# Kernel tuning notes

Measured on AMD Instinct MI355X. Metric: run time of the kernel, lower is better.

## Reference

```python
import jax, jax.numpy as jnp
import numpy as np

H = 1024  # latent_dim / GRU hidden size


def setup_inputs() -> dict:
    key = jax.random.key(0)
    ks = jax.random.split(key, 7)
    B, T, E, V = 16, 256, 512, 32000
    return {
        "latent_samples": jax.random.normal(ks[0], (B, H), jnp.float32),
        "true_outputs": jax.random.normal(ks[1], (B, T, E), jnp.float32),
        "gru_kernel": jax.random.normal(ks[2], (E, 3 * H), jnp.float32) * 0.02,
        "gru_rec_kernel": jax.random.normal(ks[3], (H, 3 * H), jnp.float32) * 0.02,
        "gru_bias": jax.random.normal(ks[4], (2, 3 * H), jnp.float32) * 0.02,
        "dense_w": jax.random.normal(ks[5], (H, V), jnp.float32) * 0.02,
        "dense_b": jax.random.normal(ks[6], (V,), jnp.float32) * 0.02,
    }


def reference(latent_samples, true_outputs, gru_kernel, gru_rec_kernel, gru_bias, dense_w, dense_b):
    # teacher_forcing_decode: GRU over true_outputs[:, :-1, :] with initial state latent_samples,
    # then TimeDistributed Dense to vocab logits. Keras GRU, reset_after=True, gate order z|r|h.
    teacher = true_outputs[:, :-1, :]                      # [B, T-1, E]
    # Precompute all input projections at once: [B, T-1, 3H]
    x_proj = jnp.einsum('bte,eg->btg', teacher, gru_kernel) + gru_bias[0]
    rec_bias = gru_bias[1]

    def step(h, x_t):  # h: [B,H], x_t: [B,3H]
        rec = h @ gru_rec_kernel + rec_bias              # [B,3H]
        xz, xr, xh = jnp.split(x_t, 3, axis=-1)
        rz, rr, rh = jnp.split(rec, 3, axis=-1)
        z = jax.nn.sigmoid(xz + rz)
        r = jax.nn.sigmoid(xr + rr)
        hh = jnp.tanh(xh + r * rh)
        h_new = z * h + (1.0 - z) * hh
        return h_new, h_new

    _, hs = jax.lax.scan(step, latent_samples, jnp.swapaxes(x_proj, 0, 1))  # hs: [T-1, B, H]
    gru_out = jnp.swapaxes(hs, 0, 1)                       # [B, T-1, H]
    logits = jnp.einsum('bth,hv->btv', gru_out, dense_w) + dense_b
    return logits
```

## Files before the change

kernel.cpp:

```cpp
#include <hip/hip_runtime.h>


typedef __attribute__((ext_vector_type(8))) short s16x8;
typedef __attribute__((ext_vector_type(4))) float f32x4;
typedef __attribute__((ext_vector_type(4))) int   i32x4;

#define B_      16
#define TSTEPS  255
#define H_      1024
#define G_      3072
#define E_      512
#define V_      32000
#define MROWS   4080
#define MPAD    4096
#define NBLK_SCAN 64
#define NWORK     448
#define NBLK_TOT  512
#define NTILE_RB  32
#define NTILE_CB  250
#define FSTRIDE   16
#define NCOPY     8
#define HCPY      16384

__device__ __forceinline__ short f2bf(float f) {
  unsigned u = __float_as_uint(f);
  u = (u + 0x7fffu + ((u >> 16) & 1u)) >> 16;
  return (short)u;
}

__device__ __forceinline__ float frcp(float x) {
  float r;
  asm("v_rcp_f32 %0, %1" : "=v"(r) : "v"(x));
  return r;
}

#define GLD_SC(dst, p)                                                         \
  asm volatile("global_load_dwordx4 %0, %1, off sc0 sc1"                       \
               : "=v"(dst) : "v"(p) : "memory")

__device__ __forceinline__ void gload_lds16(const short* g, void* l) {
  __builtin_amdgcn_global_load_lds((const __attribute__((address_space(1))) void*)g,
                                   (__attribute__((address_space(3))) void*)l,
                                   16, 0, 0);
}


__global__ void transpose_cvt(const float* __restrict__ src, short* __restrict__ dst,
                              int K, int N) {
  __shared__ float tile[32][33];
  const int n0 = blockIdx.x * 32, k0 = blockIdx.y * 32;
  const int tx = threadIdx.x, ty0 = threadIdx.y;
#pragma unroll
  for (int yy = 0; yy < 4; ++yy) {
    int ty = ty0 + yy * 8;
    tile[ty][tx] = src[(size_t)(k0 + ty) * N + (n0 + tx)];
  }
  __syncthreads();
#pragma unroll
  for (int yy = 0; yy < 4; ++yy) {
    int ty = ty0 + yy * 8;
    dst[(size_t)(n0 + ty) * K + (k0 + tx)] = f2bf(tile[tx][ty]);
  }
}

__global__ void pack_teacher(const float* __restrict__ src, short* __restrict__ dst) {
  int idx = blockIdx.x * 256 + threadIdx.x;
  int row = idx >> 6;
  int c8 = (idx & 63) << 3;
  int t = row >> 4, b = row & 15;
  s16x8 v = {};
  if (t < TSTEPS) {
    const float* s = src + ((size_t)(b * 256 + t)) * E_ + c8;
#pragma unroll
    for (int j = 0; j < 8; ++j) v[j] = f2bf(s[j]);
  }
  *(s16x8*)(dst + (size_t)row * E_ + c8) = v;
}

__global__ void init_h(const float* __restrict__ latent, short* __restrict__ hb) {
  int i = blockIdx.x * 256 + threadIdx.x;
  const short v = f2bf(latent[i]);
#pragma unroll
  for (int cp = 0; cp < NCOPY; ++cp) hb[cp * HCPY + i] = v;
}

__global__ __launch_bounds__(256) void gemm_bf16(
    const short* __restrict__ A, const short* __restrict__ BT,
    const float* __restrict__ bias, float* __restrict__ C, int N, int K) {
  const int tid = threadIdx.x;
  const int lane = tid & 63, w = tid >> 6;
  const int r = lane & 15, q = lane >> 4;
  const int bm = blockIdx.y * 128, bn = blockIdx.x * 128;
  const int wm = bm + (w >> 1) * 64, wn = bn + (w & 1) * 64;
  const short* Ab = A + (size_t)(wm + r) * K + q * 8;
  const short* Bb = BT + (size_t)(wn + r) * K + q * 8;
  f32x4 acc[4][4] = {};
  s16x8 a0[4], b0[4], a1[4], b1[4];
  const int nk = K >> 5;
#define GL(AA, BB, kk)                                                         \
  {                                                                            \
    _Pragma("unroll") for (int i = 0; i < 4; ++i) {                            \
      AA[i] = *(const s16x8*)(Ab + (size_t)i * 16 * K + (kk) * 32);            \
    }                                                                          \
    _Pragma("unroll") for (int j = 0; j < 4; ++j) {                            \
      BB[j] = *(const s16x8*)(Bb + (size_t)j * 16 * K + (kk) * 32);            \
    }                                                                          \
  }
#define MM(AA, BB)                                                             \
  {                                                                            \
    _Pragma("unroll") for (int i = 0; i < 4; ++i)                              \
        _Pragma("unroll") for (int j = 0; j < 4; ++j)                          \
            acc[i][j] = __builtin_amdgcn_mfma_f32_16x16x32_bf16(               \
                AA[i], BB[j], acc[i][j], 0, 0, 0);                             \
  }
  GL(a0, b0, 0)
#pragma unroll 1
  for (int ks = 0; ks < nk; ks += 2) {
    GL(a1, b1, ks + 1)
    MM(a0, b0)
    if (ks + 2 < nk) GL(a0, b0, ks + 2)
    MM(a1, b1)
  }
#undef GL
#undef MM
#pragma unroll
  for (int j = 0; j < 4; ++j) {
    const int col = wn + j * 16 + r;
    const float bv = bias[col];
#pragma unroll
    for (int i = 0; i < 4; ++i) {
#pragma unroll
      for (int rr = 0; rr < 4; ++rr) {
        const int row = wm + i * 16 + q * 4 + rr;
        C[(size_t)row * N + col] = acc[i][j][rr] + bv;
      }
    }
  }
}

__global__ __launch_bounds__(256, 2) void fused_scan_gemm(
    const short* __restrict__ WrecT,
    const float* __restrict__ xproj,
    const float* __restrict__ bias1,
    const float* __restrict__ latent,
    short* __restrict__ hbuf,
    short* __restrict__ gruout,
    const short* __restrict__ DwT,
    const float* __restrict__ db,
    float* __restrict__ out,
    unsigned* __restrict__ sync) {
  const int tid = threadIdx.x, lane = tid & 63, w = tid >> 6;
  const int r = lane & 15, q = lane >> 4;
  __shared__ s16x8 smem_v[2048];
  unsigned* scanflag = sync;
  unsigned* frontier = sync + NCOPY * 1024;

  if (blockIdx.x < NBLK_SCAN) {
    __builtin_amdgcn_s_setprio(3);
    float (*red)[3][64][4] = (float(*)[3][64][4])smem_v;
    const int c = blockIdx.x;
    const int cp = c & 7;
    s16x8 wb[3][8];
#pragma unroll
    for (int g = 0; g < 3; ++g)
#pragma unroll
      for (int s = 0; s < 8; ++s)
        wb[g][s] = *(const s16x8*)(WrecT + (size_t)(g * 1024 + c * 16 + r) * 1024 +
                                   (w * 8 + s) * 32 + q * 8);

    const int m = tid >> 4, nl = tid & 15, col = c * 16 + nl;
    float h = latent[m * 1024 + col];
    const float bz = bias1[col], brr = bias1[1024 + col], bhh = bias1[2048 + col];
    const float* xb = xproj + (size_t)m * G_;
    float xz = xb[col], xr = xb[1024 + col], xh = xb[2048 + col];

    for (int t = 0; t < TSTEPS; ++t) {
      const short* hcur = hbuf + ((size_t)((t & 1) * NCOPY + cp)) * HCPY;
      unsigned* hnxt = (unsigned*)(hbuf + (size_t)((t & 1) ^ 1) * NCOPY * HCPY);
      i32x4 afi[8];
#pragma unroll
      for (int s = 0; s < 8; ++s)
        GLD_SC(afi[s], hcur + r * 1024 + (w * 8 + s) * 32 + q * 8);
      asm volatile("s_waitcnt vmcnt(0)"
                   : "+v"(afi[0]), "+v"(afi[1]), "+v"(afi[2]), "+v"(afi[3]),
                     "+v"(afi[4]), "+v"(afi[5]), "+v"(afi[6]), "+v"(afi[7])
                   :: "memory");
      __builtin_amdgcn_sched_barrier(0);
      f32x4 acc[3] = {};
#pragma unroll
      for (int s = 0; s < 8; ++s) {
        const s16x8 af = *(const s16x8*)&afi[s];
        acc[0] = __builtin_amdgcn_mfma_f32_16x16x32_bf16(af, wb[0][s], acc[0], 0, 0, 0);
        acc[1] = __builtin_amdgcn_mfma_f32_16x16x32_bf16(af, wb[1][s], acc[1], 0, 0, 0);
        acc[2] = __builtin_amdgcn_mfma_f32_16x16x32_bf16(af, wb[2][s], acc[2], 0, 0, 0);
      }
      *(f32x4*)&red[w][0][lane][0] = acc[0];
      *(f32x4*)&red[w][1][lane][0] = acc[1];
      *(f32x4*)&red[w][2][lane][0] = acc[2];
      __syncthreads();
      const int rl = (m >> 2) * 16 + nl, ri = m & 3;
      float rz = bz, rr2 = brr, rh = bhh;
#pragma unroll
      for (int ww = 0; ww < 4; ++ww) {
        rz += red[ww][0][rl][ri];
        rr2 += red[ww][1][rl][ri];
        rh += red[ww][2][rl][ri];
      }
      const float z = frcp(1.f + __expf(-(xz + rz)));
      const float rg = frcp(1.f + __expf(-(xr + rr2)));
      const float hh = tanhf(xh + rg * rh);
      h = z * h + (1.f - z) * hh;
      const unsigned hb16 = (unsigned short)f2bf(h);
      const unsigned nb = __shfl(hb16, lane | 1, 64);
      const unsigned pv = hb16 | (nb << 16);
      const unsigned hoff = (unsigned)((m * 1024 + col) >> 1);
      if (!(tid & 1)) {
#pragma unroll
        for (int cp2 = 0; cp2 < NCOPY; ++cp2)
          __hip_atomic_store(hnxt + cp2 * (HCPY / 2) + hoff, pv,
                             __ATOMIC_RELAXED, __HIP_MEMORY_SCOPE_AGENT);
      }
      __syncthreads();
      if (tid == 0) {
#pragma unroll
        for (int cp2 = 0; cp2 < NCOPY; ++cp2)
          __hip_atomic_store(&scanflag[cp2 * 1024 + c * FSTRIDE], (unsigned)(t + 1),
                             __ATOMIC_RELAXED, __HIP_MEMORY_SCOPE_AGENT);
      }
      if (!(tid & 1))
        __hip_atomic_store((unsigned*)gruout + (((size_t)(t * 16 + m)) * 1024 + col) / 2,
                           pv, __ATOMIC_RELAXED, __HIP_MEMORY_SCOPE_AGENT);
      if ((t & 7) == 7) {
        asm volatile("s_waitcnt vmcnt(0)" ::: "memory");
        __syncthreads();
        if (tid == 0)
          __hip_atomic_store(&frontier[c * FSTRIDE], (unsigned)(t + 1),
                             __ATOMIC_RELAXED, __HIP_MEMORY_SCOPE_AGENT);
      }
      {
        const float* xn = xb + (size_t)(t + 1) * 16 * G_;
        xz = xn[col]; xr = xn[1024 + col]; xh = xn[2048 + col];
      }
      if (t < TSTEPS - 1) {
        const unsigned* fp = &scanflag[cp * 1024 + lane * FSTRIDE];
        unsigned v = __hip_atomic_load(fp, __ATOMIC_RELAXED,
                                       __HIP_MEMORY_SCOPE_AGENT);
        while (!__all(v > (unsigned)t))
          v = __hip_atomic_load(fp, __ATOMIC_RELAXED, __HIP_MEMORY_SCOPE_AGENT);
      }
    }
    asm volatile("s_waitcnt vmcnt(0)" ::: "memory");
    __syncthreads();
    if (tid == 0)
      __hip_atomic_store(&frontier[c * FSTRIDE], 256u,
                         __ATOMIC_RELAXED, __HIP_MEMORY_SCOPE_AGENT);
  } else {
    char* sb = (char*)smem_v;
    const int wr = w >> 1, wc = w & 1;
    const int xterm = ((q ^ ((r >> 1) & 3)) << 4);
    const int swz8 = (((lane & 3) ^ ((lane >> 3) & 3)) << 3);
    const int j = blockIdx.x - NBLK_SCAN;
#pragma unroll 1
    for (int tq = j; tq < NTILE_RB * NTILE_CB; tq += NWORK) {
      const int rb = tq / NTILE_CB, cb = tq - rb * NTILE_CB;
      const unsigned need = (unsigned)(rb < 31 ? 8 * rb + 8 : 256);
      unsigned v = __hip_atomic_load(&frontier[lane * FSTRIDE], __ATOMIC_RELAXED,
                                     __HIP_MEMORY_SCOPE_AGENT);
      while (!__all(v >= need)) {
        __builtin_amdgcn_s_sleep(32);
        v = __hip_atomic_load(&frontier[lane * FSTRIDE], __ATOMIC_RELAXED,
                              __HIP_MEMORY_SCOPE_AGENT);
      }
      const short* Ag = gruout + (size_t)rb * 128 * 1024;
      const short* Bg = DwT + (size_t)cb * 128 * 1024;
      f32x4 acc[4][4] = {};
#define STAGE(buf, kk)                                                         \
  {                                                                            \
    _Pragma("unroll") for (int it = 0; it < 2; ++it) {                         \
      const size_t go = (size_t)(w * 32 + it * 16 + (lane >> 2)) * 1024 +      \
                        (kk) * 32 + swz8;                                      \
      char* lb2 = sb + (buf) * 16384 + w * 2048 + it * 1024;                   \
      gload_lds16(Ag + go, lb2);                                               \
      gload_lds16(Bg + go, lb2 + 8192);                                        \
    }                                                                          \
  }
      STAGE(0, 0)
#pragma unroll 1
      for (int kk = 0; kk < 32; ++kk) {
        __syncthreads();
        if (kk < 31) STAGE((kk + 1) & 1, kk + 1)
        const char* ab = sb + (kk & 1) * 16384;
        s16x8 af[4], bf[4];
#pragma unroll
        for (int i = 0; i < 4; ++i)
          af[i] = *(const s16x8*)(ab + (wr * 64 + i * 16 + r) * 64 + xterm);
#pragma unroll
        for (int j5 = 0; j5 < 4; ++j5)
          bf[j5] = *(const s16x8*)(ab + 8192 + (wc * 64 + j5 * 16 + r) * 64 + xterm);
#pragma unroll
        for (int i = 0; i < 4; ++i)
#pragma unroll
          for (int j5 = 0; j5 < 4; ++j5)
            acc[i][j5] = __builtin_amdgcn_mfma_f32_16x16x32_bf16(
                af[i], bf[j5], acc[i][j5], 0, 0, 0);
      }
#undef STAGE
      const int wm = rb * 128 + wr * 64, wn = cb * 128 + wc * 64;
#pragma unroll
      for (int j2 = 0; j2 < 4; ++j2) {
        const int col = wn + j2 * 16 + r;
        const float bv = db[col];
#pragma unroll
        for (int i = 0; i < 4; ++i) {
#pragma unroll
          for (int rr = 0; rr < 4; ++rr) {
            const int arow = wm + i * 16 + q * 4 + rr;
            const int t = arow >> 4, mm = arow & 15;
            if (t < TSTEPS)
              __builtin_nontemporal_store(
                  acc[i][j2][rr] + bv,
                  &out[(size_t)(mm * TSTEPS + t) * V_ + col]);
          }
        }
      }
      __syncthreads();
    }
  }
}

extern "C" void kernel_launch(void* const* d_in, const int* in_sizes, int n_in,
                              void* d_out, int out_size, void* d_ws, size_t ws_size,
                              hipStream_t stream) {
  const float* latent = (const float*)d_in[0];
  const float* trueo  = (const float*)d_in[1];
  const float* gk     = (const float*)d_in[2];
  const float* grk    = (const float*)d_in[3];
  const float* gbias  = (const float*)d_in[4];
  const float* dw     = (const float*)d_in[5];
  const float* db     = (const float*)d_in[6];
  float* out = (float*)d_out;
  char* ws = (char*)d_ws;
  short*    WrecT  = (short*)(ws + 0);
  short*    GkT    = (short*)(ws + 6291456);
  short*    DwT    = (short*)(ws + 9437184);
  short*    teachA = (short*)(ws + 74973184);
  short*    hbuf   = (short*)(ws + 74973184);
  unsigned* syncb  = (unsigned*)(ws + 75497472);
  float*    xproj  = (float*)(ws + 79167488);
  short*    gruout = (short*)(ws + 129499136);

  transpose_cvt<<<dim3(96, 32), dim3(32, 8), 0, stream>>>(grk, WrecT, 1024, 3072);
  transpose_cvt<<<dim3(96, 16), dim3(32, 8), 0, stream>>>(gk, GkT, 512, 3072);
  transpose_cvt<<<dim3(1000, 32), dim3(32, 8), 0, stream>>>(dw, DwT, 1024, 32000);
  pack_teacher<<<1024, 256, 0, stream>>>(trueo, teachA);
  gemm_bf16<<<dim3(24, 32), 256, 0, stream>>>(teachA, GkT, gbias, xproj, G_, E_);
  hipMemsetAsync(syncb, 0, 36864, stream);
  init_h<<<64, 256, 0, stream>>>(latent, hbuf);
  fused_scan_gemm<<<NBLK_TOT, 256, 0, stream>>>(WrecT, xproj, gbias + G_, latent,
                                                hbuf, gruout, DwT, db, out, syncb);
}
```

Before: 980.3 us.

## Replace replicated ping-pong hidden-state buffers with a single write-once history buffer

The scan blocks now write each step's hidden state once, to a unique slot in a [T+1,B,H] history buffer. This replaces fanning out to eight replicated ping-pong copies plus eight flag copies and a separate gruout write. Because every address is written only once before it is read, the per-step h loads drop the sc0 sc1 cache-bypass bits, and the logits GEMM reads its A operand straight from the history. The goal is to cut per-step store traffic and latency in the serial recurrence. In exchange, the waitcnt/barrier before publishing the frontier flag is removed, which risks the GEMM blocks seeing the flag before the history writes are visible.

```diff
diff --git a/kernel.cpp b/kernel.cpp
--- a/kernel.cpp
+++ b/kernel.cpp
@@ -19,8 +19,6 @@
 #define NTILE_RB  32
 #define NTILE_CB  250
 #define FSTRIDE   16
-#define NCOPY     8
-#define HCPY      16384
 
 __device__ __forceinline__ short f2bf(float f) {
   unsigned u = __float_as_uint(f);
@@ -34,8 +32,8 @@
   return r;
 }
 
-#define GLD_SC(dst, p)                                                         \
-  asm volatile("global_load_dwordx4 %0, %1, off sc0 sc1"                       \
+#define GLD_C(dst, p)                                                          \
+  asm volatile("global_load_dwordx4 %0, %1, off"                               \
                : "=v"(dst) : "v"(p) : "memory")
 
 __device__ __forceinline__ void gload_lds16(const short* g, void* l) {
@@ -77,11 +75,9 @@
   *(s16x8*)(dst + (size_t)row * E_ + c8) = v;
 }
 
-__global__ void init_h(const float* __restrict__ latent, short* __restrict__ hb) {
+__global__ void init_h(const float* __restrict__ latent, short* __restrict__ hist) {
   int i = blockIdx.x * 256 + threadIdx.x;
-  const short v = f2bf(latent[i]);
-#pragma unroll
-  for (int cp = 0; cp < NCOPY; ++cp) hb[cp * HCPY + i] = v;
+  hist[i] = f2bf(latent[i]);
 }
 
 __global__ __launch_bounds__(256) void gemm_bf16(
@@ -143,8 +139,7 @@
     const float* __restrict__ xproj,
     const float* __restrict__ bias1,
     const float* __restrict__ latent,
-    short* __restrict__ hbuf,
-    short* __restrict__ gruout,
+    short* __restrict__ hist,
     const short* __restrict__ DwT,
     const float* __restrict__ db,
     float* __restrict__ out,
@@ -153,13 +148,12 @@
   const int r = lane & 15, q = lane >> 4;
   __shared__ s16x8 smem_v[2048];
   unsigned* scanflag = sync;
-  unsigned* frontier = sync + NCOPY * 1024;
+  unsigned* frontier = sync + 1024;
 
   if (blockIdx.x < NBLK_SCAN) {
     __builtin_amdgcn_s_setprio(3);
     float (*red)[3][64][4] = (float(*)[3][64][4])smem_v;
     const int c = blockIdx.x;
-    const int cp = c & 7;
     s16x8 wb[3][8];
 #pragma unroll
     for (int g = 0; g < 3; ++g)
@@ -175,12 +169,10 @@
     float xz = xb[col], xr = xb[1024 + col], xh = xb[2048 + col];
 
     for (int t = 0; t < TSTEPS; ++t) {
-      const short* hcur = hbuf + ((size_t)((t & 1) * NCOPY + cp)) * HCPY;
-      unsigned* hnxt = (unsigned*)(hbuf + (size_t)((t & 1) ^ 1) * NCOPY * HCPY);
+      const short* hrow = hist + ((size_t)t * 16 + r) * 1024 + w * 256 + q * 8;
       i32x4 afi[8];
 #pragma unroll
-      for (int s = 0; s < 8; ++s)
-        GLD_SC(afi[s], hcur + r * 1024 + (w * 8 + s) * 32 + q * 8);
+      for (int s = 0; s < 8; ++s) GLD_C(afi[s], hrow + s * 32);
       asm volatile("s_waitcnt vmcnt(0)"
                    : "+v"(afi[0]), "+v"(afi[1]), "+v"(afi[2]), "+v"(afi[3]),
                      "+v"(afi[4]), "+v"(afi[5]), "+v"(afi[6]), "+v"(afi[7])
@@ -213,26 +205,15 @@
       const unsigned hb16 = (unsigned short)f2bf(h);
       const unsigned nb = __shfl(hb16, lane | 1, 64);
       const unsigned pv = hb16 | (nb << 16);
-      const unsigned hoff = (unsigned)((m * 1024 + col) >> 1);
-      if (!(tid & 1)) {
-#pragma unroll
-        for (int cp2 = 0; cp2 < NCOPY; ++cp2)
-          __hip_atomic_store(hnxt + cp2 * (HCPY / 2) + hoff, pv,
-                             __ATOMIC_RELAXED, __HIP_MEMORY_SCOPE_AGENT);
-      }
+      if (!(tid & 1))
+        __hip_atomic_store(
+            (unsigned*)hist + (((size_t)(t + 1) * 16 + m) * 1024 + col) / 2,
+            pv, __ATOMIC_RELAXED, __HIP_MEMORY_SCOPE_AGENT);
       __syncthreads();
-      if (tid == 0) {
-#pragma unroll
-        for (int cp2 = 0; cp2 < NCOPY; ++cp2)
-          __hip_atomic_store(&scanflag[cp2 * 1024 + c * FSTRIDE], (unsigned)(t + 1),
-                             __ATOMIC_RELAXED, __HIP_MEMORY_SCOPE_AGENT);
-      }
-      if (!(tid & 1))
-        __hip_atomic_store((unsigned*)gruout + (((size_t)(t * 16 + m)) * 1024 + col) / 2,
-                           pv, __ATOMIC_RELAXED, __HIP_MEMORY_SCOPE_AGENT);
+      if (tid == 0)
+        __hip_atomic_store(&scanflag[c * FSTRIDE], (unsigned)(t + 1),
+                           __ATOMIC_RELAXED, __HIP_MEMORY_SCOPE_AGENT);
       if ((t & 7) == 7) {
-        asm volatile("s_waitcnt vmcnt(0)" ::: "memory");
-        __syncthreads();
         if (tid == 0)
           __hip_atomic_store(&frontier[c * FSTRIDE], (unsigned)(t + 1),
                              __ATOMIC_RELAXED, __HIP_MEMORY_SCOPE_AGENT);
@@ -242,15 +223,13 @@
         xz = xn[col]; xr = xn[1024 + col]; xh = xn[2048 + col];
       }
       if (t < TSTEPS - 1) {
-        const unsigned* fp = &scanflag[cp * 1024 + lane * FSTRIDE];
+        const unsigned* fp = &scanflag[lane * FSTRIDE];
         unsigned v = __hip_atomic_load(fp, __ATOMIC_RELAXED,
                                        __HIP_MEMORY_SCOPE_AGENT);
         while (!__all(v > (unsigned)t))
           v = __hip_atomic_load(fp, __ATOMIC_RELAXED, __HIP_MEMORY_SCOPE_AGENT);
       }
     }
-    asm volatile("s_waitcnt vmcnt(0)" ::: "memory");
-    __syncthreads();
     if (tid == 0)
       __hip_atomic_store(&frontier[c * FSTRIDE], 256u,
                          __ATOMIC_RELAXED, __HIP_MEMORY_SCOPE_AGENT);
@@ -271,7 +250,7 @@
         v = __hip_atomic_load(&frontier[lane * FSTRIDE], __ATOMIC_RELAXED,
                               __HIP_MEMORY_SCOPE_AGENT);
       }
-      const short* Ag = gruout + (size_t)rb * 128 * 1024;
+      const short* Ag = hist + (size_t)16 * 1024 + (size_t)rb * 128 * 1024;
       const short* Bg = DwT + (size_t)cb * 128 * 1024;
       f32x4 acc[4][4] = {};
 #define STAGE(buf, kk)                                                         \
@@ -344,18 +323,17 @@
   short*    GkT    = (short*)(ws + 6291456);
   short*    DwT    = (short*)(ws + 9437184);
   short*    teachA = (short*)(ws + 74973184);
-  short*    hbuf   = (short*)(ws + 74973184);
-  unsigned* syncb  = (unsigned*)(ws + 75497472);
   float*    xproj  = (float*)(ws + 79167488);
-  short*    gruout = (short*)(ws + 129499136);
-
+  short*    hist   = (short*)(ws + 129499136);
+  unsigned* syncb  = (unsigned*)(ws + 137920512);
+
+  hipMemsetAsync(syncb, 0, 8192, stream);
   transpose_cvt<<<dim3(96, 32), dim3(32, 8), 0, stream>>>(grk, WrecT, 1024, 3072);
   transpose_cvt<<<dim3(96, 16), dim3(32, 8), 0, stream>>>(gk, GkT, 512, 3072);
   transpose_cvt<<<dim3(1000, 32), dim3(32, 8), 0, stream>>>(dw, DwT, 1024, 32000);
   pack_teacher<<<1024, 256, 0, stream>>>(trueo, teachA);
   gemm_bf16<<<dim3(24, 32), 256, 0, stream>>>(teachA, GkT, gbias, xproj, G_, E_);
-  hipMemsetAsync(syncb, 0, 36864, stream);
-  init_h<<<64, 256, 0, stream>>>(latent, hbuf);
+  init_h<<<64, 256, 0, stream>>>(latent, hist);
   fused_scan_gemm<<<NBLK_TOT, 256, 0, stream>>>(WrecT, xproj, gbias + G_, latent,
-                                                hbuf, gruout, DwT, db, out, syncb);
-}
+                                                hist, DwT, db, out, syncb);
+}
```

New measurement: 923.8 us, median of 2. -5.8%, faster.
